# Kernel optimization log

Hardware: AMD Instinct MI355X
Metric: run time of the kernel (lower is better)

## Reference

```python
import jax, jax.numpy as jnp
import numpy as np

KSZ = 7
PAD = 3


def setup_inputs() -> dict:
    key = jax.random.key(0)
    ks = jax.random.split(key, 5)
    b, t, c, h, w = 8, 16, 256, 28, 28
    x = jax.random.normal(ks[0], (b, t, c, h, w), dtype=jnp.float32)
    W1 = jax.random.normal(ks[1], (2 * t, t), dtype=jnp.float32) * 0.1
    W2 = jax.random.normal(ks[2], (KSZ, 2 * t), dtype=jnp.float32) * 0.1
    Wl1 = jax.random.normal(ks[3], (c // 4, c, KSZ), dtype=jnp.float32) * 0.05
    Wl2 = jax.random.normal(ks[4], (c, c // 4, 1), dtype=jnp.float32) * 0.1
    return {"x": x, "W1": W1, "W2": W2, "Wl1": Wl1, "Wl2": Wl2}


def _tam_forward(x, W1, W2, Wl1, Wl2):
    b, t, c, h, w = x.shape
    xp = jnp.transpose(x, (0, 2, 1, 3, 4))  # [b,c,t,h,w]
    pooled = jnp.mean(xp, axis=(3, 4))       # [b,c,t] (adaptive_avg_pool2d to 1x1)

    # G branch: per-(b,c) dynamic 7-tap softmax kernel
    g = jnp.tanh(jnp.einsum('bct,ut->bcu', pooled, W1))
    kernel = jax.nn.softmax(jnp.einsum('bcu,ku->bck', g, W2), axis=-1)  # [b,c,7]

    # L branch: conv1d(c -> c/4, k=7, pad=3) -> tanh -> conv1d(c/4 -> c, k=1) -> sigmoid
    y = jax.lax.conv_general_dilated(
        pooled, Wl1, window_strides=(1,), padding=[(PAD, PAD)],
        dimension_numbers=('NCH', 'OIH', 'NCH'))
    y = jnp.tanh(y)  # [b, c/4, t]
    local = jax.nn.sigmoid(jnp.einsum('oi,bit->bot', Wl2[:, :, 0], y))  # [b,c,t]

    gated = xp * local[:, :, :, None, None]  # [b,c,t,h,w]

    # Depthwise temporal conv (groups = b*c), stride 1, pad 3 on t
    padded = jnp.pad(gated, ((0, 0), (0, 0), (PAD, PAD), (0, 0), (0, 0)))
    out = jnp.zeros_like(gated)
    for k in range(KSZ):
        out = out + kernel[:, :, k, None, None, None] * padded[:, :, k:k + t]
    out = jnp.transpose(out, (0, 2, 1, 3, 4))  # [b,t,c,h,w]
    return out.reshape(b * t, c, h, w)


def reference(x, W1, W2, Wl1, Wl2):
    return _tam_forward(x, W1, W2, Wl1, Wl2)
```

## Files before the change

### kernel.cpp

```cpp
#include <hip/hip_runtime.h>

constexpr int B_  = 8;
constexpr int T_  = 16;
constexpr int C_  = 256;
constexpr int HW_ = 784;
constexpr int CO_ = 64;
constexpr int K_  = 7;
constexpr int U2_ = 32;

typedef float floatx4 __attribute__((ext_vector_type(4)));

__device__ __forceinline__ float rfl(float v) {
    return __int_as_float(__builtin_amdgcn_readfirstlane(__float_as_int(v)));
}

__global__ __launch_bounds__(256) void pool_kernel(const float* __restrict__ x,
                                                   float* __restrict__ pooled) {
    int bid  = blockIdx.x;
    int cg   = bid & 63;
    int bt   = bid >> 6;
    int t    = bt & 15;
    int b    = bt >> 4;
    int wave = threadIdx.x >> 6;
    int lane = threadIdx.x & 63;
    int c    = cg * 4 + wave;

    const float4* p4 = (const float4*)(x + ((size_t)bt * C_ + c) * HW_);
    float s = 0.f;
    for (int j = lane; j < 196; j += 64) {
        float4 v = p4[j];
        s += (v.x + v.y) + (v.z + v.w);
    }
#pragma unroll
    for (int m = 32; m >= 1; m >>= 1) s += __shfl_xor(s, m, 64);
    if (lane == 0) pooled[((size_t)b * C_ + c) * T_ + t] = s * (1.0f / 784.0f);
}

__global__ __launch_bounds__(256) void ty_kernel(const float* __restrict__ pooled,
                                                 const float* __restrict__ Wl1,
                                                 float* __restrict__ ty) {
    int b = blockIdx.x / CO_;
    int o = blockIdx.x % CO_;
    __shared__ float pld[T_ * 257];

    int tid = threadIdx.x;
    for (int idx = tid; idx < C_ * T_; idx += 256) {
        int i  = idx >> 4;
        int tt = idx & 15;
        pld[tt * 257 + i] = pooled[((size_t)b * C_ + i) * T_ + tt];
    }
    __syncthreads();

    int t = tid >> 4;
    int q = tid & 15;
    const float* wrow = Wl1 + (size_t)o * (C_ * K_);
    float acc = 0.f;
    for (int j = 0; j < 16; ++j) {
        int i = j * 16 + q;
        const float* wp = wrow + i * K_;
#pragma unroll
        for (int k = 0; k < K_; ++k) {
            int tt = t + k - 3;
            if (tt >= 0 && tt < T_) acc += wp[k] * pld[tt * 257 + i];
        }
    }
    acc += __shfl_xor(acc, 1, 64);
    acc += __shfl_xor(acc, 2, 64);
    acc += __shfl_xor(acc, 4, 64);
    acc += __shfl_xor(acc, 8, 64);
    if (q == 0) ty[((size_t)b * CO_ + o) * T_ + t] = tanhf(acc);
}

__global__ __launch_bounds__(64) void abuild_kernel(const float* __restrict__ pooled,
                                                    const float* __restrict__ ty,
                                                    const float* __restrict__ W1,
                                                    const float* __restrict__ W2,
                                                    const float* __restrict__ Wl2,
                                                    float* __restrict__ P) {
    int bc = blockIdx.x;
    int b  = bc >> 8;
    int c  = bc & 255;
    int lane = threadIdx.x;

    __shared__ float g_s[U2_];
    __shared__ float s_s[K_];
    __shared__ float loc_s[T_];
    __shared__ float kw_s[8];

    {
        int t = lane >> 2, q = lane & 3;
        float acc = 0.f;
#pragma unroll
        for (int jj = 0; jj < 16; ++jj) {
            int i = q * 16 + jj;
            acc += Wl2[(size_t)c * CO_ + i] * ty[((size_t)b * CO_ + i) * T_ + t];
        }
        acc += __shfl_xor(acc, 1, 64);
        acc += __shfl_xor(acc, 2, 64);
        if (q == 0) loc_s[t] = 1.0f / (1.0f + __expf(-acc));
    }
    if (lane < U2_) {
        float acc = 0.f;
#pragma unroll
        for (int t2 = 0; t2 < T_; ++t2)
            acc += pooled[((size_t)b * C_ + c) * T_ + t2] * W1[lane * T_ + t2];
        g_s[lane] = tanhf(acc);
    }
    __syncthreads();
    if (lane < K_) {
        float acc = 0.f;
#pragma unroll
        for (int u = 0; u < U2_; ++u) acc += g_s[u] * W2[lane * U2_ + u];
        s_s[lane] = acc;
    }
    __syncthreads();
    if (lane == 0) {
        float m = s_s[0];
#pragma unroll
        for (int k = 1; k < K_; ++k) m = fmaxf(m, s_s[k]);
        float e[K_], sum = 0.f;
#pragma unroll
        for (int k = 0; k < K_; ++k) { e[k] = __expf(s_s[k] - m); sum += e[k]; }
        float inv = 1.0f / sum;
#pragma unroll
        for (int k = 0; k < K_; ++k) kw_s[k] = e[k] * inv;
        kw_s[7] = 0.f;
    }
    __syncthreads();
    float* row = P + (size_t)bc * 32;
    if (lane < 8)                 row[lane] = kw_s[lane];
    if (lane >= 8 && lane < 24)   row[lane] = loc_s[lane - 8];
}

__global__ __launch_bounds__(256, 8) void stream_kernel(const float* __restrict__ x,
                                                        const float* __restrict__ P,
                                                        float* __restrict__ out) {
    int bc = blockIdx.x;
    int b  = bc >> 8;
    int c  = bc & 255;
    int col = threadIdx.x;

    const float* row = P + (size_t)bc * 32;
    float kw[K_];
    float lc[T_];
#pragma unroll
    for (int k = 0; k < K_; ++k) kw[k] = rfl(row[k]);
#pragma unroll
    for (int t = 0; t < T_; ++t) lc[t] = rfl(row[8 + t]);

    if (col >= 196) return;

    const size_t chan = ((size_t)b * T_ * C_ + c) * HW_ + (size_t)col * 4;
    const float* xb = x + chan;
    float*       ob = out + chan;
    const size_t ts = (size_t)C_ * HW_;

    floatx4 w[11];
#pragma unroll
    for (int tp = 0; tp < 11; ++tp)
        w[tp] = *(const floatx4*)(xb + (size_t)tp * ts) * lc[tp];

#pragma unroll
    for (int t = 0; t < 8; ++t) {
        floatx4 acc = {0.f, 0.f, 0.f, 0.f};
#pragma unroll
        for (int d = -3; d <= 3; ++d) {
            int tp = t + d;
            if (tp >= 0 && tp <= 10) acc += kw[d + 3] * w[tp];
        }
        __builtin_nontemporal_store(acc, (floatx4*)(ob + (size_t)t * ts));
    }

    floatx4 w2[11];
#pragma unroll
    for (int j = 0; j < 6; ++j) w2[j] = w[5 + j];
#pragma unroll
    for (int tp = 11; tp < 16; ++tp)
        w2[tp - 5] = *(const floatx4*)(xb + (size_t)tp * ts) * lc[tp];

#pragma unroll
    for (int t = 8; t < 16; ++t) {
        floatx4 acc = {0.f, 0.f, 0.f, 0.f};
#pragma unroll
        for (int d = -3; d <= 3; ++d) {
            int tp = t + d;
            if (tp <= 15) acc += kw[d + 3] * w2[tp - 5];
        }
        __builtin_nontemporal_store(acc, (floatx4*)(ob + (size_t)t * ts));
    }
}

extern "C" void kernel_launch(void* const* d_in, const int* in_sizes, int n_in,
                              void* d_out, int out_size, void* d_ws, size_t ws_size,
                              hipStream_t stream) {
    const float* x   = (const float*)d_in[0];
    const float* W1  = (const float*)d_in[1];
    const float* W2  = (const float*)d_in[2];
    const float* Wl1 = (const float*)d_in[3];
    const float* Wl2 = (const float*)d_in[4];
    float* out = (float*)d_out;

    float* pooled = (float*)d_ws;
    float* ty     = pooled + B_ * C_ * T_;
    float* P      = ty + B_ * CO_ * T_;

    pool_kernel<<<B_ * T_ * (C_ / 4), 256, 0, stream>>>(x, pooled);
    ty_kernel<<<B_ * CO_, 256, 0, stream>>>(pooled, Wl1, ty);
    abuild_kernel<<<B_ * C_, 64, 0, stream>>>(pooled, ty, W1, W2, Wl2, P);
    stream_kernel<<<B_ * C_, 256, 0, stream>>>(x, P, out);
}
```

Baseline: 72.99 us.

## Fuse all four stages into one cooperative persistent kernel with grid syncs

Replaces the pool, ty, abuild and stream kernels with one cooperative kernel that runs persistent blocks and separates the phases with grid.sync(). The kernel-build step is folded into the streaming loop, so the P workspace buffer and three launch boundaries are dropped. Pooling is reorganised so each block handles one (b,c) channel across all 16 time steps. Costs: grid-wide barriers, a grid capped at 1024 blocks, extra shared-memory barriers per channel, and two full reads of x that are no longer split across a kernel boundary.

```diff
diff --git a/kernel.cpp b/kernel.cpp
--- a/kernel.cpp
+++ b/kernel.cpp
@@ -1,4 +1,7 @@
 #include <hip/hip_runtime.h>
+#include <hip/hip_cooperative_groups.h>
+
+namespace cg = cooperative_groups;
 
 constexpr int B_  = 8;
 constexpr int T_  = 16;
@@ -7,6 +10,8 @@
 constexpr int CO_ = 64;
 constexpr int K_  = 7;
 constexpr int U2_ = 32;
+constexpr int NCH = B_ * C_;
+constexpr int NTY = B_ * CO_;
 
 typedef float floatx4 __attribute__((ext_vector_type(4)));
 
@@ -14,179 +19,162 @@
     return __int_as_float(__builtin_amdgcn_readfirstlane(__float_as_int(v)));
 }
 
-__global__ __launch_bounds__(256) void pool_kernel(const float* __restrict__ x,
-                                                   float* __restrict__ pooled) {
-    int bid  = blockIdx.x;
-    int cg   = bid & 63;
-    int bt   = bid >> 6;
-    int t    = bt & 15;
-    int b    = bt >> 4;
-    int wave = threadIdx.x >> 6;
-    int lane = threadIdx.x & 63;
-    int c    = cg * 4 + wave;
-
-    const float4* p4 = (const float4*)(x + ((size_t)bt * C_ + c) * HW_);
-    float s = 0.f;
-    for (int j = lane; j < 196; j += 64) {
-        float4 v = p4[j];
-        s += (v.x + v.y) + (v.z + v.w);
+__global__ __launch_bounds__(256, 4)
+void tam_fused(const float* __restrict__ x,  const float* __restrict__ W1,
+               const float* __restrict__ W2, const float* __restrict__ Wl1,
+               const float* __restrict__ Wl2, float* __restrict__ out,
+               float* __restrict__ pooled,    float* __restrict__ ty) {
+    cg::grid_group grid = cg::this_grid();
+    const int g   = blockIdx.x;
+    const int G   = gridDim.x;
+    const int tid = threadIdx.x;
+    const int wave = tid >> 6, lane = tid & 63;
+    const size_t ts = (size_t)C_ * HW_;
+
+    __shared__ float pld[T_ * 257];
+    __shared__ float pool_s[T_];
+    __shared__ float g_s[U2_];
+    __shared__ float s_s[8];
+    __shared__ float kw_s[8];
+    __shared__ float loc_s[T_];
+
+    for (int bc = g; bc < NCH; bc += G) {
+        int b = bc >> 8, c = bc & 255;
+        const float* xc = x + ((size_t)(b * T_) * C_ + c) * HW_;
+#pragma unroll
+        for (int j = 0; j < 4; ++j) {
+            int t = wave * 4 + j;
+            const floatx4* p4 = (const floatx4*)(xc + (size_t)t * ts);
+            float s = 0.f;
+            for (int col = lane; col < 196; col += 64) {
+                floatx4 v = p4[col];
+                s += (v.x + v.y) + (v.z + v.w);
+            }
+#pragma unroll
+            for (int m = 32; m >= 1; m >>= 1) s += __shfl_xor(s, m, 64);
+            if (lane == 0) pooled[(size_t)bc * T_ + t] = s * (1.0f / 784.0f);
+        }
     }
-#pragma unroll
-    for (int m = 32; m >= 1; m >>= 1) s += __shfl_xor(s, m, 64);
-    if (lane == 0) pooled[((size_t)b * C_ + c) * T_ + t] = s * (1.0f / 784.0f);
-}
-
-__global__ __launch_bounds__(256) void ty_kernel(const float* __restrict__ pooled,
-                                                 const float* __restrict__ Wl1,
-                                                 float* __restrict__ ty) {
-    int b = blockIdx.x / CO_;
-    int o = blockIdx.x % CO_;
-    __shared__ float pld[T_ * 257];
-
-    int tid = threadIdx.x;
-    for (int idx = tid; idx < C_ * T_; idx += 256) {
-        int i  = idx >> 4;
-        int tt = idx & 15;
-        pld[tt * 257 + i] = pooled[((size_t)b * C_ + i) * T_ + tt];
-    }
-    __syncthreads();
-
-    int t = tid >> 4;
-    int q = tid & 15;
-    const float* wrow = Wl1 + (size_t)o * (C_ * K_);
-    float acc = 0.f;
-    for (int j = 0; j < 16; ++j) {
-        int i = j * 16 + q;
-        const float* wp = wrow + i * K_;
-#pragma unroll
-        for (int k = 0; k < K_; ++k) {
-            int tt = t + k - 3;
-            if (tt >= 0 && tt < T_) acc += wp[k] * pld[tt * 257 + i];
-        }
-    }
-    acc += __shfl_xor(acc, 1, 64);
-    acc += __shfl_xor(acc, 2, 64);
-    acc += __shfl_xor(acc, 4, 64);
-    acc += __shfl_xor(acc, 8, 64);
-    if (q == 0) ty[((size_t)b * CO_ + o) * T_ + t] = tanhf(acc);
-}
-
-__global__ __launch_bounds__(64) void abuild_kernel(const float* __restrict__ pooled,
-                                                    const float* __restrict__ ty,
-                                                    const float* __restrict__ W1,
-                                                    const float* __restrict__ W2,
-                                                    const float* __restrict__ Wl2,
-                                                    float* __restrict__ P) {
-    int bc = blockIdx.x;
-    int b  = bc >> 8;
-    int c  = bc & 255;
-    int lane = threadIdx.x;
-
-    __shared__ float g_s[U2_];
-    __shared__ float s_s[K_];
-    __shared__ float loc_s[T_];
-    __shared__ float kw_s[8];
-
-    {
-        int t = lane >> 2, q = lane & 3;
+    grid.sync();
+
+    for (int u = g; u < NTY; u += G) {
+        int b = u / CO_, o = u % CO_;
+        for (int idx = tid; idx < C_ * T_; idx += 256) {
+            int i = idx >> 4, tt = idx & 15;
+            pld[tt * 257 + i] = pooled[((size_t)b * C_ + i) * T_ + tt];
+        }
+        __syncthreads();
+        int t = tid >> 4, q = tid & 15;
+        const float* wrow = Wl1 + (size_t)o * (C_ * K_);
         float acc = 0.f;
-#pragma unroll
-        for (int jj = 0; jj < 16; ++jj) {
-            int i = q * 16 + jj;
-            acc += Wl2[(size_t)c * CO_ + i] * ty[((size_t)b * CO_ + i) * T_ + t];
+        for (int jm = 0; jm < 16; ++jm) {
+            int i = jm * 16 + q;
+            const float* wp = wrow + i * K_;
+#pragma unroll
+            for (int k = 0; k < K_; ++k) {
+                int tt = t + k - 3;
+                if (tt >= 0 && tt < T_) acc += wp[k] * pld[tt * 257 + i];
+            }
         }
         acc += __shfl_xor(acc, 1, 64);
         acc += __shfl_xor(acc, 2, 64);
-        if (q == 0) loc_s[t] = 1.0f / (1.0f + __expf(-acc));
+        acc += __shfl_xor(acc, 4, 64);
+        acc += __shfl_xor(acc, 8, 64);
+        if (q == 0) ty[(size_t)u * T_ + t] = tanhf(acc);
+        __syncthreads();
     }
-    if (lane < U2_) {
-        float acc = 0.f;
-#pragma unroll
-        for (int t2 = 0; t2 < T_; ++t2)
-            acc += pooled[((size_t)b * C_ + c) * T_ + t2] * W1[lane * T_ + t2];
-        g_s[lane] = tanhf(acc);
-    }
-    __syncthreads();
-    if (lane < K_) {
-        float acc = 0.f;
-#pragma unroll
-        for (int u = 0; u < U2_; ++u) acc += g_s[u] * W2[lane * U2_ + u];
-        s_s[lane] = acc;
-    }
-    __syncthreads();
-    if (lane == 0) {
-        float m = s_s[0];
-#pragma unroll
-        for (int k = 1; k < K_; ++k) m = fmaxf(m, s_s[k]);
-        float e[K_], sum = 0.f;
-#pragma unroll
-        for (int k = 0; k < K_; ++k) { e[k] = __expf(s_s[k] - m); sum += e[k]; }
-        float inv = 1.0f / sum;
-#pragma unroll
-        for (int k = 0; k < K_; ++k) kw_s[k] = e[k] * inv;
-        kw_s[7] = 0.f;
-    }
-    __syncthreads();
-    float* row = P + (size_t)bc * 32;
-    if (lane < 8)                 row[lane] = kw_s[lane];
-    if (lane >= 8 && lane < 24)   row[lane] = loc_s[lane - 8];
-}
-
-__global__ __launch_bounds__(256, 8) void stream_kernel(const float* __restrict__ x,
-                                                        const float* __restrict__ P,
-                                                        float* __restrict__ out) {
-    int bc = blockIdx.x;
-    int b  = bc >> 8;
-    int c  = bc & 255;
-    int col = threadIdx.x;
-
-    const float* row = P + (size_t)bc * 32;
-    float kw[K_];
-    float lc[T_];
-#pragma unroll
-    for (int k = 0; k < K_; ++k) kw[k] = rfl(row[k]);
-#pragma unroll
-    for (int t = 0; t < T_; ++t) lc[t] = rfl(row[8 + t]);
-
-    if (col >= 196) return;
-
-    const size_t chan = ((size_t)b * T_ * C_ + c) * HW_ + (size_t)col * 4;
-    const float* xb = x + chan;
-    float*       ob = out + chan;
-    const size_t ts = (size_t)C_ * HW_;
-
-    floatx4 w[11];
-#pragma unroll
-    for (int tp = 0; tp < 11; ++tp)
-        w[tp] = *(const floatx4*)(xb + (size_t)tp * ts) * lc[tp];
-
-#pragma unroll
-    for (int t = 0; t < 8; ++t) {
-        floatx4 acc = {0.f, 0.f, 0.f, 0.f};
-#pragma unroll
-        for (int d = -3; d <= 3; ++d) {
-            int tp = t + d;
-            if (tp >= 0 && tp <= 10) acc += kw[d + 3] * w[tp];
-        }
-        __builtin_nontemporal_store(acc, (floatx4*)(ob + (size_t)t * ts));
-    }
-
-    floatx4 w2[11];
-#pragma unroll
-    for (int j = 0; j < 6; ++j) w2[j] = w[5 + j];
-#pragma unroll
-    for (int tp = 11; tp < 16; ++tp)
-        w2[tp - 5] = *(const floatx4*)(xb + (size_t)tp * ts) * lc[tp];
-
-#pragma unroll
-    for (int t = 8; t < 16; ++t) {
-        floatx4 acc = {0.f, 0.f, 0.f, 0.f};
-#pragma unroll
-        for (int d = -3; d <= 3; ++d) {
-            int tp = t + d;
-            if (tp <= 15) acc += kw[d + 3] * w2[tp - 5];
-        }
-        __builtin_nontemporal_store(acc, (floatx4*)(ob + (size_t)t * ts));
+    grid.sync();
+
+    for (int bc = g; bc < NCH; bc += G) {
+        int b = bc >> 8, c = bc & 255;
+
+        {
+            int t = tid >> 4, q = tid & 15;
+            float acc = 0.f;
+#pragma unroll
+            for (int jj = 0; jj < 4; ++jj) {
+                int o = q + jj * 16;
+                acc += Wl2[(size_t)c * CO_ + o] * ty[((size_t)b * CO_ + o) * T_ + t];
+            }
+            acc += __shfl_xor(acc, 1, 64);
+            acc += __shfl_xor(acc, 2, 64);
+            acc += __shfl_xor(acc, 4, 64);
+            acc += __shfl_xor(acc, 8, 64);
+            if (q == 0) loc_s[t] = 1.0f / (1.0f + __expf(-acc));
+        }
+        if (tid < T_) pool_s[tid] = pooled[(size_t)bc * T_ + tid];
+        __syncthreads();
+        if (tid < U2_) {
+            float acc = 0.f;
+#pragma unroll
+            for (int t2 = 0; t2 < T_; ++t2) acc += pool_s[t2] * W1[tid * T_ + t2];
+            g_s[tid] = tanhf(acc);
+        }
+        __syncthreads();
+        if (tid < K_) {
+            float acc = 0.f;
+#pragma unroll
+            for (int u2 = 0; u2 < U2_; ++u2) acc += g_s[u2] * W2[tid * U2_ + u2];
+            s_s[tid] = acc;
+        }
+        __syncthreads();
+        if (tid == 0) {
+            float m = s_s[0];
+#pragma unroll
+            for (int k = 1; k < K_; ++k) m = fmaxf(m, s_s[k]);
+            float e[K_], sum = 0.f;
+#pragma unroll
+            for (int k = 0; k < K_; ++k) { e[k] = __expf(s_s[k] - m); sum += e[k]; }
+            float inv = 1.0f / sum;
+#pragma unroll
+            for (int k = 0; k < K_; ++k) kw_s[k] = e[k] * inv;
+        }
+        __syncthreads();
+
+        float kw[K_], lc[T_];
+#pragma unroll
+        for (int k = 0; k < K_; ++k) kw[k] = rfl(kw_s[k]);
+#pragma unroll
+        for (int t = 0; t < T_; ++t) lc[t] = rfl(loc_s[t]);
+        __syncthreads();
+
+        if (tid < 196) {
+            const size_t chan = ((size_t)(b * T_) * C_ + c) * HW_ + (size_t)tid * 4;
+            const float* xb = x + chan;
+            float*       ob = out + chan;
+
+            floatx4 w[11];
+#pragma unroll
+            for (int tp = 0; tp < 11; ++tp)
+                w[tp] = *(const floatx4*)(xb + (size_t)tp * ts) * lc[tp];
+#pragma unroll
+            for (int t = 0; t < 8; ++t) {
+                floatx4 acc = {0.f, 0.f, 0.f, 0.f};
+#pragma unroll
+                for (int d = -3; d <= 3; ++d) {
+                    int tp = t + d;
+                    if (tp >= 0 && tp <= 10) acc += kw[d + 3] * w[tp];
+                }
+                __builtin_nontemporal_store(acc, (floatx4*)(ob + (size_t)t * ts));
+            }
+
+            floatx4 w2[11];
+#pragma unroll
+            for (int j = 0; j < 6; ++j) w2[j] = w[5 + j];
+#pragma unroll
+            for (int tp = 11; tp < 16; ++tp)
+                w2[tp - 5] = *(const floatx4*)(xb + (size_t)tp * ts) * lc[tp];
+#pragma unroll
+            for (int t = 8; t < 16; ++t) {
+                floatx4 acc = {0.f, 0.f, 0.f, 0.f};
+#pragma unroll
+                for (int d = -3; d <= 3; ++d) {
+                    int tp = t + d;
+                    if (tp <= 15) acc += kw[d + 3] * w2[tp - 5];
+                }
+                __builtin_nontemporal_store(acc, (floatx4*)(ob + (size_t)t * ts));
+            }
+        }
     }
 }
 
@@ -201,11 +189,17 @@
     float* out = (float*)d_out;
 
     float* pooled = (float*)d_ws;
-    float* ty     = pooled + B_ * C_ * T_;
-    float* P      = ty + B_ * CO_ * T_;
-
-    pool_kernel<<<B_ * T_ * (C_ / 4), 256, 0, stream>>>(x, pooled);
-    ty_kernel<<<B_ * CO_, 256, 0, stream>>>(pooled, Wl1, ty);
-    abuild_kernel<<<B_ * C_, 64, 0, stream>>>(pooled, ty, W1, W2, Wl2, P);
-    stream_kernel<<<B_ * C_, 256, 0, stream>>>(x, P, out);
+    float* ty     = pooled + NCH * T_;
+
+    int blocksPerCU = 0;
+    hipOccupancyMaxActiveBlocksPerMultiprocessor(&blocksPerCU,
+        (const void*)tam_fused, 256, 0);
+    if (blocksPerCU < 1) blocksPerCU = 1;
+    int grid = blocksPerCU * 256;
+    if (grid > 1024) grid = 1024;
+
+    void* args[] = { (void*)&x, (void*)&W1, (void*)&W2, (void*)&Wl1,
+                     (void*)&Wl2, (void*)&out, (void*)&pooled, (void*)&ty };
+    hipLaunchCooperativeKernel((const void*)tam_fused, dim3(grid), dim3(256),
+                               args, 0, stream);
 }
```

Measured after the change: 186.7 us. 156% more time.

## Stage fp16 copy of x during pooling and stream from it

Applied to the files above, without the earlier changes.

The pooling kernel now also writes a half-precision copy of x, laid out per (b,c) channel with t contiguous. The temporal conv stream kernel reads this fp16 copy instead of fp32 x, halving its read traffic and improving locality. The cost is an extra 51MB write in the pool pass and fp16 rounding of the input. The path is used only when the workspace is large enough, otherwise it falls back to the fp32 kernel.

```diff
diff --git a/kernel.cpp b/kernel.cpp
--- a/kernel.cpp
+++ b/kernel.cpp
@@ -8,14 +8,16 @@
 constexpr int K_  = 7;
 constexpr int U2_ = 32;
 
-typedef float floatx4 __attribute__((ext_vector_type(4)));
+typedef float    floatx4 __attribute__((ext_vector_type(4)));
+typedef _Float16 half4   __attribute__((ext_vector_type(4)));
 
 __device__ __forceinline__ float rfl(float v) {
     return __int_as_float(__builtin_amdgcn_readfirstlane(__float_as_int(v)));
 }
 
-__global__ __launch_bounds__(256) void pool_kernel(const float* __restrict__ x,
-                                                   float* __restrict__ pooled) {
+__global__ __launch_bounds__(256) void pool_cvt_kernel(const float* __restrict__ x,
+                                                       float* __restrict__ pooled,
+                                                       _Float16* __restrict__ x16) {
     int bid  = blockIdx.x;
     int cg   = bid & 63;
     int bt   = bid >> 6;
@@ -25,11 +27,14 @@
     int lane = threadIdx.x & 63;
     int c    = cg * 4 + wave;
 
-    const float4* p4 = (const float4*)(x + ((size_t)bt * C_ + c) * HW_);
+    const floatx4* p4 = (const floatx4*)(x + ((size_t)bt * C_ + c) * HW_);
+    half4* d4 = x16 ? (half4*)(x16 + ((size_t)(b * C_ + c) * T_ + t) * HW_) : nullptr;
+
     float s = 0.f;
     for (int j = lane; j < 196; j += 64) {
-        float4 v = p4[j];
+        floatx4 v = p4[j];
         s += (v.x + v.y) + (v.z + v.w);
+        if (d4) d4[j] = __builtin_convertvector(v, half4);
     }
 #pragma unroll
     for (int m = 32; m >= 1; m >>= 1) s += __shfl_xor(s, m, 64);
@@ -132,17 +137,16 @@
     if (lane >= 8 && lane < 24)   row[lane] = loc_s[lane - 8];
 }
 
-__global__ __launch_bounds__(256, 8) void stream_kernel(const float* __restrict__ x,
-                                                        const float* __restrict__ P,
-                                                        float* __restrict__ out) {
+__global__ __launch_bounds__(256) void stream16_kernel(const _Float16* __restrict__ x16,
+                                                       const float* __restrict__ P,
+                                                       float* __restrict__ out) {
     int bc = blockIdx.x;
     int b  = bc >> 8;
     int c  = bc & 255;
     int col = threadIdx.x;
 
     const float* row = P + (size_t)bc * 32;
-    float kw[K_];
-    float lc[T_];
+    float kw[K_], lc[T_];
 #pragma unroll
     for (int k = 0; k < K_; ++k) kw[k] = rfl(row[k]);
 #pragma unroll
@@ -150,7 +154,65 @@
 
     if (col >= 196) return;
 
-    const size_t chan = ((size_t)b * T_ * C_ + c) * HW_ + (size_t)col * 4;
+    const _Float16* xb = x16 + (size_t)bc * T_ * HW_ + (size_t)col * 4;
+    float* ob = out + ((size_t)(b * T_) * C_ + c) * HW_ + (size_t)col * 4;
+    const size_t ts = (size_t)C_ * HW_;
+
+    floatx4 w[11];
+#pragma unroll
+    for (int tp = 0; tp < 11; ++tp) {
+        half4 h = *(const half4*)(xb + tp * HW_);
+        w[tp] = __builtin_convertvector(h, floatx4) * lc[tp];
+    }
+#pragma unroll
+    for (int t = 0; t < 8; ++t) {
+        floatx4 acc = {0.f, 0.f, 0.f, 0.f};
+#pragma unroll
+        for (int d = -3; d <= 3; ++d) {
+            int tp = t + d;
+            if (tp >= 0 && tp <= 10) acc += kw[d + 3] * w[tp];
+        }
+        __builtin_nontemporal_store(acc, (floatx4*)(ob + (size_t)t * ts));
+    }
+
+    floatx4 w2[11];
+#pragma unroll
+    for (int j = 0; j < 6; ++j) w2[j] = w[5 + j];
+#pragma unroll
+    for (int tp = 11; tp < 16; ++tp) {
+        half4 h = *(const half4*)(xb + tp * HW_);
+        w2[tp - 5] = __builtin_convertvector(h, floatx4) * lc[tp];
+    }
+#pragma unroll
+    for (int t = 8; t < 16; ++t) {
+        floatx4 acc = {0.f, 0.f, 0.f, 0.f};
+#pragma unroll
+        for (int d = -3; d <= 3; ++d) {
+            int tp = t + d;
+            if (tp <= 15) acc += kw[d + 3] * w2[tp - 5];
+        }
+        __builtin_nontemporal_store(acc, (floatx4*)(ob + (size_t)t * ts));
+    }
+}
+
+__global__ __launch_bounds__(256) void stream_kernel(const float* __restrict__ x,
+                                                     const float* __restrict__ P,
+                                                     float* __restrict__ out) {
+    int bc = blockIdx.x;
+    int b  = bc >> 8;
+    int c  = bc & 255;
+    int col = threadIdx.x;
+
+    const float* row = P + (size_t)bc * 32;
+    float kw[K_], lc[T_];
+#pragma unroll
+    for (int k = 0; k < K_; ++k) kw[k] = rfl(row[k]);
+#pragma unroll
+    for (int t = 0; t < T_; ++t) lc[t] = rfl(row[8 + t]);
+
+    if (col >= 196) return;
+
+    const size_t chan = ((size_t)(b * T_) * C_ + c) * HW_ + (size_t)col * 4;
     const float* xb = x + chan;
     float*       ob = out + chan;
     const size_t ts = (size_t)C_ * HW_;
@@ -159,7 +221,6 @@
 #pragma unroll
     for (int tp = 0; tp < 11; ++tp)
         w[tp] = *(const floatx4*)(xb + (size_t)tp * ts) * lc[tp];
-
 #pragma unroll
     for (int t = 0; t < 8; ++t) {
         floatx4 acc = {0.f, 0.f, 0.f, 0.f};
@@ -170,14 +231,12 @@
         }
         __builtin_nontemporal_store(acc, (floatx4*)(ob + (size_t)t * ts));
     }
-
     floatx4 w2[11];
 #pragma unroll
     for (int j = 0; j < 6; ++j) w2[j] = w[5 + j];
 #pragma unroll
     for (int tp = 11; tp < 16; ++tp)
         w2[tp - 5] = *(const floatx4*)(xb + (size_t)tp * ts) * lc[tp];
-
 #pragma unroll
     for (int t = 8; t < 16; ++t) {
         floatx4 acc = {0.f, 0.f, 0.f, 0.f};
@@ -203,9 +262,16 @@
     float* pooled = (float*)d_ws;
     float* ty     = pooled + B_ * C_ * T_;
     float* P      = ty + B_ * CO_ * T_;
-
-    pool_kernel<<<B_ * T_ * (C_ / 4), 256, 0, stream>>>(x, pooled);
+    size_t head_bytes = (size_t)(32768 + 8192 + 65536) * 4;
+    _Float16* x16 = (_Float16*)((char*)d_ws + head_bytes);
+    size_t need = head_bytes + (size_t)B_ * C_ * T_ * HW_ * sizeof(_Float16);
+    bool use16 = (ws_size >= need);
+
+    pool_cvt_kernel<<<B_ * T_ * (C_ / 4), 256, 0, stream>>>(x, pooled, use16 ? x16 : nullptr);
     ty_kernel<<<B_ * CO_, 256, 0, stream>>>(pooled, Wl1, ty);
     abuild_kernel<<<B_ * C_, 64, 0, stream>>>(pooled, ty, W1, W2, Wl2, P);
-    stream_kernel<<<B_ * C_, 256, 0, stream>>>(x, P, out);
-}
+    if (use16)
+        stream16_kernel<<<B_ * C_, 256, 0, stream>>>(x16, P, out);
+    else
+        stream_kernel<<<B_ * C_, 256, 0, stream>>>(x, P, out);
+}
```

Result: no change. 74.26 us (+1.7%).
